# Kernel tuning notes

Measured on AMD Instinct MI355X. Metric: run time of the kernel, lower is better.

Reference implementation:

```python
import jax, jax.numpy as jnp
import numpy as np

B, T, C = 2, 2048, 1024
H = 16
DH = C // H  # 64
DFF = 4 * C  # 4096
EPS = 1e-5


def layernorm(x, gamma, beta):
    # torch.var defaults to unbiased (ddof=1) -- replicate exactly
    m = jnp.mean(x, axis=-1, keepdims=True)
    v = jnp.var(x, axis=-1, ddof=1, keepdims=True)
    return (x - m) / jnp.sqrt(v + EPS) * gamma + beta


def setup_inputs() -> dict:
    key = jax.random.key(0)
    ks = jax.random.split(key, 12)
    s = 0.02
    return {
        "x": jax.random.normal(ks[0], (B, T, C), jnp.float32),
        "Wq": jax.random.normal(ks[1], (H, C, DH), jnp.float32) * s,
        "bq": jnp.zeros((H, DH), jnp.float32),
        "Wk": jax.random.normal(ks[2], (H, C, DH), jnp.float32) * s,
        "bk": jnp.zeros((H, DH), jnp.float32),
        "Wv": jax.random.normal(ks[3], (H, C, DH), jnp.float32) * s,
        "bv": jnp.zeros((H, DH), jnp.float32),
        "Wo": jax.random.normal(ks[4], (C, C), jnp.float32) * s,
        "bo": jnp.zeros((C,), jnp.float32),
        "gamma1": jnp.ones((C,), jnp.float32),
        "beta1": jnp.zeros((C,), jnp.float32),
        "gamma2": jnp.ones((C,), jnp.float32),
        "beta2": jnp.zeros((C,), jnp.float32),
        "W1": jax.random.normal(ks[5], (C, DFF), jnp.float32) * s,
        "b1": jnp.zeros((DFF,), jnp.float32),
        "W2": jax.random.normal(ks[6], (DFF, C), jnp.float32) * s,
        "b2": jnp.zeros((C,), jnp.float32),
    }


def reference(x, Wq, bq, Wk, bk, Wv, bv, Wo, bo,
              gamma1, beta1, gamma2, beta2, W1, b1, W2, b2):
    Tn = x.shape[1]
    # Block: x = ln1(x); x = x + attn(x); x = ln2(x); out = x + ffw(x)
    x = layernorm(x, gamma1, beta1)

    # per-head Q/K/V linears, stacked over heads: [B,T,C] x [H,C,Dh] -> [B,H,T,Dh]
    q = jnp.einsum('btc,hcd->bhtd', x, Wq) + bq[None, :, None, :]
    k = jnp.einsum('btc,hcd->bhtd', x, Wk) + bk[None, :, None, :]
    v = jnp.einsum('btc,hcd->bhtd', x, Wv) + bv[None, :, None, :]

    scale = DH ** -0.5
    scores = jnp.einsum('bhtd,bhsd->bhts', q, k) * scale  # [B,H,T,T]
    causal = jnp.tril(jnp.ones((Tn, Tn), dtype=bool))
    scores = jnp.where(causal, scores, -jnp.inf)
    alpha = jax.nn.softmax(scores, axis=-1)
    h = jnp.einsum('bhts,bhsd->bhtd', alpha, v)  # [B,H,T,Dh]
    h = jnp.transpose(h, (0, 2, 1, 3)).reshape(x.shape)  # concat heads -> [B,T,C]
    attn_out = h @ Wo + bo

    x = x + attn_out
    x = layernorm(x, gamma2, beta2)
    ffw = jax.nn.gelu(x @ W1 + b1, approximate=False) @ W2 + b2
    return x + ffw
```

## Files before the change

### kernel.cpp

```cpp
#include <hip/hip_runtime.h>

typedef unsigned short u16;
typedef unsigned int u32;
typedef __attribute__((ext_vector_type(8))) short bf16x8;
typedef __attribute__((ext_vector_type(4))) float f32x4;

#define AS1 __attribute__((address_space(1)))
#define AS3 __attribute__((address_space(3)))

__device__ __forceinline__ u16 f2bf(float f) {
  u32 u = __float_as_uint(f);
  u = (u + 0x7fffu + ((u >> 16) & 1u)) >> 16;
  return (u16)u;
}
__device__ __forceinline__ float bf2f(u16 v) { return __uint_as_float((u32)v << 16); }

__device__ __forceinline__ void gl16(const void* g, void* l) {
  __builtin_amdgcn_global_load_lds((AS1 void*)g, (AS3 void*)l, 16, 0, 0);
}

__device__ __forceinline__ float exp2a(float x) {
  float r;
  asm("v_exp_f32 %0, %1" : "=v"(r) : "v"(x));
  return r;
}
__device__ __forceinline__ u32 pk2(float lo, float hi) {
  u32 r;
  asm("v_cvt_pk_bf16_f32 %0, %1, %2" : "=v"(r) : "v"(lo), "v"(hi));
  return r;
}

#define LGKM0()                                         \
  do {                                                  \
    asm volatile("s_waitcnt lgkmcnt(0)" ::: "memory");  \
    __builtin_amdgcn_sched_barrier(0);                  \
  } while (0)
#define VMC0()                                          \
  do {                                                  \
    asm volatile("s_waitcnt vmcnt(0)" ::: "memory");    \
    __builtin_amdgcn_sched_barrier(0);                  \
  } while (0)

__global__ __launch_bounds__(256) void ln_kernel(const float* __restrict__ in,
                                                 const float* __restrict__ gamma,
                                                 const float* __restrict__ beta,
                                                 u16* __restrict__ obf,
                                                 float* __restrict__ of32) {
  const int row = blockIdx.x;
  const int tid = threadIdx.x;
  const float* xr = in + (long)row * 1024;
  float4 v = *(const float4*)(xr + tid * 4);
  float s = v.x + v.y + v.z + v.w;
  float sq = v.x * v.x + v.y * v.y + v.z * v.z + v.w * v.w;
#pragma unroll
  for (int off = 1; off < 64; off <<= 1) {
    s += __shfl_xor(s, off);
    sq += __shfl_xor(sq, off);
  }
  __shared__ float rs[4], rq[4];
  const int w = tid >> 6, lane = tid & 63;
  if (lane == 0) { rs[w] = s; rq[w] = sq; }
  __syncthreads();
  s = rs[0] + rs[1] + rs[2] + rs[3];
  sq = rq[0] + rq[1] + rq[2] + rq[3];
  const float mean = s * (1.0f / 1024.0f);
  const float var = (sq - 1024.0f * mean * mean) * (1.0f / 1023.0f);
  const float rstd = rsqrtf(var + 1e-5f);
  float4 g4 = *(const float4*)(gamma + tid * 4);
  float4 b4 = *(const float4*)(beta + tid * 4);
  float o0 = (v.x - mean) * rstd * g4.x + b4.x;
  float o1 = (v.y - mean) * rstd * g4.y + b4.y;
  float o2 = (v.z - mean) * rstd * g4.z + b4.z;
  float o3 = (v.w - mean) * rstd * g4.w + b4.w;
  *(float4*)(of32 + (long)row * 1024 + tid * 4) = make_float4(o0, o1, o2, o3);
  ushort4 ub;
  ub.x = f2bf(o0); ub.y = f2bf(o1); ub.z = f2bf(o2); ub.w = f2bf(o3);
  *(ushort4*)(obf + (long)row * 1024 + tid * 4) = ub;
}

__global__ __launch_bounds__(256) void ln2_fused_kernel(
    const u16* __restrict__ p0, const u16* __restrict__ p1,
    const float* __restrict__ bo, const float* __restrict__ xn,
    const float* __restrict__ gamma, const float* __restrict__ beta,
    u16* __restrict__ obf, float* __restrict__ of32) {
  const int row = blockIdx.x;
  const int tid = threadIdx.x;
  const long i4 = (long)row * 1024 + tid * 4;
  ushort4 a0 = *(const ushort4*)(p0 + i4);
  ushort4 a1 = *(const ushort4*)(p1 + i4);
  float4 xv = *(const float4*)(xn + i4);
  float4 bv = *(const float4*)(bo + tid * 4);
  float y0 = bf2f(a0.x) + bf2f(a1.x) + bv.x + xv.x;
  float y1 = bf2f(a0.y) + bf2f(a1.y) + bv.y + xv.y;
  float y2 = bf2f(a0.z) + bf2f(a1.z) + bv.z + xv.z;
  float y3 = bf2f(a0.w) + bf2f(a1.w) + bv.w + xv.w;
  float s = y0 + y1 + y2 + y3;
  float sq = y0 * y0 + y1 * y1 + y2 * y2 + y3 * y3;
#pragma unroll
  for (int off = 1; off < 64; off <<= 1) {
    s += __shfl_xor(s, off);
    sq += __shfl_xor(sq, off);
  }
  __shared__ float rs[4], rq[4];
  const int w = tid >> 6, lane = tid & 63;
  if (lane == 0) { rs[w] = s; rq[w] = sq; }
  __syncthreads();
  s = rs[0] + rs[1] + rs[2] + rs[3];
  sq = rq[0] + rq[1] + rq[2] + rq[3];
  const float mean = s * (1.0f / 1024.0f);
  const float var = (sq - 1024.0f * mean * mean) * (1.0f / 1023.0f);
  const float rstd = rsqrtf(var + 1e-5f);
  float4 g4 = *(const float4*)(gamma + tid * 4);
  float4 b4 = *(const float4*)(beta + tid * 4);
  float o0 = (y0 - mean) * rstd * g4.x + b4.x;
  float o1 = (y1 - mean) * rstd * g4.y + b4.y;
  float o2 = (y2 - mean) * rstd * g4.z + b4.z;
  float o3 = (y3 - mean) * rstd * g4.w + b4.w;
  *(float4*)(of32 + i4) = make_float4(o0, o1, o2, o3);
  ushort4 ub;
  ub.x = f2bf(o0); ub.y = f2bf(o1); ub.z = f2bf(o2); ub.w = f2bf(o3);
  *(ushort4*)(obf + i4) = ub;
}

__global__ __launch_bounds__(256) void wtrans_kernel(const float* __restrict__ in,
                                                     u16* __restrict__ out,
                                                     int R, int C, int in_rs,
                                                     long in_batch, long out_batch) {
  __shared__ float tile[32][33];
  const float* ip = in + (long)blockIdx.z * in_batch;
  u16* op = out + (long)blockIdx.z * out_batch;
  const int c0 = blockIdx.x * 32, r0 = blockIdx.y * 32;
  const int tx = threadIdx.x, ty = threadIdx.y;
#pragma unroll
  for (int i = 0; i < 4; ++i)
    tile[ty + i * 8][tx] = ip[(long)(r0 + ty + i * 8) * in_rs + c0 + tx];
  __syncthreads();
#pragma unroll
  for (int i = 0; i < 4; ++i)
    op[(long)(c0 + ty + i * 8) * R + r0 + tx] = f2bf(tile[tx][ty + i * 8]);
}

__global__ __launch_bounds__(256) void ffn2_reduce_kernel(const u16* __restrict__ p,
                                                          const float* __restrict__ b2,
                                                          const float* __restrict__ yn,
                                                          float* __restrict__ out) {
  const long i4 = ((long)blockIdx.x * 256 + threadIdx.x) * 4;
  ushort4 p0 = *(const ushort4*)(p + i4);
  ushort4 p1 = *(const ushort4*)(p + 4194304 + i4);
  ushort4 p2 = *(const ushort4*)(p + 8388608 + i4);
  ushort4 p3 = *(const ushort4*)(p + 12582912 + i4);
  float4 rr = *(const float4*)(yn + i4);
  const int nn = (int)(i4 & 1023);
  float4 bb = *(const float4*)(b2 + nn);
  float4 o;
  o.x = bf2f(p0.x) + bf2f(p1.x) + bf2f(p2.x) + bf2f(p3.x) + bb.x + rr.x;
  o.y = bf2f(p0.y) + bf2f(p1.y) + bf2f(p2.y) + bf2f(p3.y) + bb.y + rr.y;
  o.z = bf2f(p0.z) + bf2f(p1.z) + bf2f(p2.z) + bf2f(p3.z) + bb.z + rr.z;
  o.w = bf2f(p0.w) + bf2f(p1.w) + bf2f(p2.w) + bf2f(p3.w) + bb.w + rr.w;
  *(float4*)(out + i4) = o;
}

template <int EPI>
__global__ __launch_bounds__(256, 2) void gemm128_kernel(
    const u16* __restrict__ A, const u16* __restrict__ Bt,
    int K, int nk, int N,
    const float* bias0, const float* bias1, const float* bias2,
    void* out0, void* out1) {
  __shared__ __align__(16) u16 Asm[128 * 64];
  __shared__ __align__(16) u16 Bsm[128 * 64];
  const int tid = threadIdx.x;
  const int lane = tid & 63, w = tid >> 6;
  const int wm = w >> 1, wn = w & 1;
  const int q = lane & 15, g = lane >> 4;
  const long m0 = (long)blockIdx.x * 128;
  const long n0 = (long)blockIdx.y * 128;
  const int bz = blockIdx.z;
  const long koff = (long)bz * (long)nk * 64;

  f32x4 zero4 = {0.f, 0.f, 0.f, 0.f};
  f32x4 acc[4][4];
#pragma unroll
  for (int mi = 0; mi < 4; ++mi)
#pragma unroll
    for (int ni = 0; ni < 4; ++ni) acc[mi][ni] = zero4;

  for (int ks = 0; ks < nk; ++ks) {
    __syncthreads();
    const u16* ga = A + m0 * K + koff + ks * 64;
    const u16* gb = Bt + n0 * K + koff + ks * 64;
    const int base = w * 256;
#pragma unroll
    for (int i = 0; i < 4; ++i) {
      const int idx = base + i * 64 + lane;
      const int row = idx >> 3;
      const int lg = (idx & 7) ^ (row & 7);
      gl16(ga + (long)row * K + lg * 8, Asm + (long)(base + i * 64) * 8);
    }
#pragma unroll
    for (int i = 0; i < 4; ++i) {
      const int idx = base + i * 64 + lane;
      const int row = idx >> 3;
      const int lg = (idx & 7) ^ (row & 7);
      gl16(gb + (long)row * K + lg * 8, Bsm + (long)(base + i * 64) * 8);
    }
    __syncthreads();
#pragma unroll
    for (int half = 0; half < 2; ++half) {
      bf16x8 af[4], bfv[4];
#pragma unroll
      for (int mi = 0; mi < 4; ++mi) {
        const int row = wm * 64 + mi * 16 + q;
        const int ph = (half * 4 + g) ^ (row & 7);
        af[mi] = *(const bf16x8*)(Asm + row * 64 + ph * 8);
      }
#pragma unroll
      for (int ni = 0; ni < 4; ++ni) {
        const int row = wn * 64 + ni * 16 + q;
        const int ph = (half * 4 + g) ^ (row & 7);
        bfv[ni] = *(const bf16x8*)(Bsm + row * 64 + ph * 8);
      }
#pragma unroll
      for (int mi = 0; mi < 4; ++mi)
#pragma unroll
        for (int ni = 0; ni < 4; ++ni)
          acc[mi][ni] = __builtin_amdgcn_mfma_f32_16x16x32_bf16(af[mi], bfv[ni],
                                                                acc[mi][ni], 0, 0, 0);
    }
  }
#pragma unroll
  for (int mi = 0; mi < 4; ++mi) {
#pragma unroll
    for (int ni = 0; ni < 4; ++ni) {
      const long mbase = m0 + wm * 64 + mi * 16 + 4 * g;
      const long n = n0 + wn * 64 + ni * 16 + q;
      f32x4 a = acc[mi][ni];
      if constexpr (EPI == 0) {
        const int sel = (int)(n >> 10);
        const int nn = (int)(n & 1023);
        const float* bp = sel == 0 ? bias0 : (sel == 1 ? bias1 : bias2);
        const float bb2 = bp[nn];
        if (sel < 2) {
          const float sc = (sel == 0) ? 0.18033688011112043f : 1.0f;
          u16* qkp = (u16*)out0;
#pragma unroll
          for (int r = 0; r < 4; ++r)
            qkp[(mbase + r) * 2048 + n] = f2bf((a[r] + bb2) * sc);
        } else {
          const int bI = (int)(mbase >> 11);
          const int t = (int)(mbase & 2047);
          const int hh = nn >> 6, dh = nn & 63;
          ushort4 pk;
          pk.x = f2bf(a[0] + bb2); pk.y = f2bf(a[1] + bb2);
          pk.z = f2bf(a[2] + bb2); pk.w = f2bf(a[3] + bb2);
          *(ushort4*)((u16*)out1 + ((long)((bI * 16 + hh) * 64 + dh)) * 2048 + t) = pk;
        }
      } else if constexpr (EPI == 2) {
        u16* gp = (u16*)out0;
        const float bb2 = bias0[(int)n];
#pragma unroll
        for (int r = 0; r < 4; ++r) {
          const float xg = a[r] + bb2;
          const float ge = 0.5f * xg * (1.0f + erff(xg * 0.70710678118f));
          gp[(mbase + r) * N + n] = f2bf(ge);
        }
      } else {
        u16* pp = (u16*)out0 + (long)bz * 4096 * 1024;
#pragma unroll
        for (int r = 0; r < 4; ++r) pp[(mbase + r) * 1024 + n] = f2bf(a[r]);
      }
    }
  }
}

__device__ __forceinline__ void attn_stage(const u16* kbase, const u16* vtb, int kb,
                                           u16* Kd, u16* Vd, int tid) {
#pragma unroll
  for (int it = 0; it < 2; ++it) {
    const int j = it * 256 + tid;
    const int row = j >> 3;
    const int lg = (j & 7) ^ (row & 7);
    gl16(kbase + (long)(kb * 64 + row) * 2048 + lg * 8, Kd + j * 8);
    gl16(vtb + (long)row * 2048 + kb * 64 + lg * 8, Vd + j * 8);
  }
}

__device__ __forceinline__ void softmax_slab(const f32x4 st[4], bool diag, int qrow,
                                             int kb, int g, int q15,
                                             float& m2, float& l, u16* prow,
                                             float al[4]) {
  float sv[4][4];
  float rmax = -1e30f;
#pragma unroll
  for (int sub = 0; sub < 4; ++sub)
#pragma unroll
    for (int r = 0; r < 4; ++r) {
      float s_ = st[sub][r];
      if (diag) {
        const int key = kb * 64 + sub * 16 + 4 * g + r;
        s_ = (key > qrow) ? -1e30f : s_;
      }
      sv[sub][r] = s_;
      rmax = fmaxf(rmax, s_);
    }
  rmax = fmaxf(rmax, __shfl_xor(rmax, 16));
  rmax = fmaxf(rmax, __shfl_xor(rmax, 32));
  const float mnew = fmaxf(m2, rmax);
  const float alpha = exp2a(m2 - mnew);
  float psum = 0.f;
#pragma unroll
  for (int sub = 0; sub < 4; ++sub) {
    const float p0 = exp2a(sv[sub][0] - mnew);
    const float p1 = exp2a(sv[sub][1] - mnew);
    const float p2 = exp2a(sv[sub][2] - mnew);
    const float p3 = exp2a(sv[sub][3] - mnew);
    uint2 u;
    u.x = pk2(p0, p1);
    u.y = pk2(p2, p3);
    *(uint2*)(prow + sub * 16 + 4 * g) = u;
    psum += (p0 + p1) + (p2 + p3);
  }
  psum += __shfl_xor(psum, 16);
  psum += __shfl_xor(psum, 32);
  l = l * alpha + psum;
  m2 = mnew;
#pragma unroll
  for (int r = 0; r < 4; ++r) al[r] = __shfl(alpha, 4 * g + r);
}

__global__ __launch_bounds__(256, 2) void attn_kernel(const u16* __restrict__ qk,
                                                      const u16* __restrict__ vT,
                                                      u16* __restrict__ o) {
  __shared__ __align__(16) u16 Ksm[2][64 * 64];
  __shared__ __align__(16) u16 Vsm[2][64 * 64];
  __shared__ __align__(16) u16 Psm[8][16][72];
  const int lid = blockIdx.x;
  const int xcd = lid & 7, s6 = lid >> 3;
  const int b2 = (s6 >> 4) & 3, xr = s6 & 15;
  const int qs = (b2 & 2) ? (15 - xr) : xr;
  const int bh = xcd + 8 * b2;
  const int b = bh >> 4, h = bh & 15;
  const int tid = threadIdx.x, lane = tid & 63, w = tid >> 6;
  const int q15 = lane & 15, g = lane >> 4;
  const u16* qbase = qk + (long)b * 2048 * 2048 + h * 64;
  const u16* kbase = qbase + 1024;
  const u16* vtb = vT + (long)bh * 64 * 2048;
  f32x4 zero4 = {0.f, 0.f, 0.f, 0.f};

  const int r0 = qs * 128 + w * 16 + q15;
  bf16x8 qa[2][2];
  qa[0][0] = *(const bf16x8*)(qbase + (long)r0 * 2048 + g * 8);
  qa[0][1] = *(const bf16x8*)(qbase + (long)r0 * 2048 + 32 + g * 8);
  qa[1][0] = *(const bf16x8*)(qbase + (long)(r0 + 64) * 2048 + g * 8);
  qa[1][1] = *(const bf16x8*)(qbase + (long)(r0 + 64) * 2048 + 32 + g * 8);

  f32x4 oa0[4], oa1[4];
#pragma unroll
  for (int dv = 0; dv < 4; ++dv) { oa0[dv] = zero4; oa1[dv] = zero4; }
  float m20 = -1e30f, l0 = 0.f, m21 = -1e30f, l1 = 0.f;
  const int kbmax = 2 * qs + 1;

  attn_stage(kbase, vtb, 0, Ksm[0], Vsm[0], tid);
  VMC0();
  __syncthreads();

  for (int kb = 0; kb <= kbmax; ++kb) {
    const int buf = kb & 1;
    if (kb < kbmax) attn_stage(kbase, vtb, kb + 1, Ksm[buf ^ 1], Vsm[buf ^ 1], tid);
    const u16* Kb = Ksm[buf];
    const u16* Vb = Vsm[buf];
    const bool s0on = (kb <= 2 * qs);
    f32x4 st0[4], st1[4];
#pragma unroll
    for (int sub = 0; sub < 4; ++sub) {
      const int row = sub * 16 + q15;
      const bf16x8 ka0 = *(const bf16x8*)(Kb + row * 64 + ((g ^ (row & 7)) * 8));
      const bf16x8 ka1 = *(const bf16x8*)(Kb + row * 64 + (((4 + g) ^ (row & 7)) * 8));
      f32x4 z = zero4;
      z = __builtin_amdgcn_mfma_f32_16x16x32_bf16(ka0, qa[1][0], z, 0, 0, 0);
      z = __builtin_amdgcn_mfma_f32_16x16x32_bf16(ka1, qa[1][1], z, 0, 0, 0);
      st1[sub] = z;
      if (s0on) {
        f32x4 z0 = zero4;
        z0 = __builtin_amdgcn_mfma_f32_16x16x32_bf16(ka0, qa[0][0], z0, 0, 0, 0);
        z0 = __builtin_amdgcn_mfma_f32_16x16x32_bf16(ka1, qa[0][1], z0, 0, 0, 0);
        st0[sub] = z0;
      }
    }
    float al0[4], al1[4];
    if (s0on)
      softmax_slab(st0, kb == 2 * qs, r0, kb, g, q15, m20, l0, &Psm[w * 2][q15][0], al0);
    softmax_slab(st1, kb == 2 * qs + 1, r0 + 64, kb, g, q15, m21, l1,
                 &Psm[w * 2 + 1][q15][0], al1);
    if (s0on)
#pragma unroll
      for (int dv = 0; dv < 4; ++dv) {
        oa0[dv][0] *= al0[0]; oa0[dv][1] *= al0[1];
        oa0[dv][2] *= al0[2]; oa0[dv][3] *= al0[3];
      }
#pragma unroll
    for (int dv = 0; dv < 4; ++dv) {
      oa1[dv][0] *= al1[0]; oa1[dv][1] *= al1[1];
      oa1[dv][2] *= al1[2]; oa1[dv][3] *= al1[3];
    }
    LGKM0();
#pragma unroll
    for (int half = 0; half < 2; ++half) {
      const bf16x8 pa0 = *(const bf16x8*)(&Psm[w * 2][q15][half * 32 + 8 * g]);
      const bf16x8 pa1 = *(const bf16x8*)(&Psm[w * 2 + 1][q15][half * 32 + 8 * g]);
#pragma unroll
      for (int dv = 0; dv < 4; ++dv) {
        const int row = dv * 16 + q15;
        const bf16x8 vb = *(const bf16x8*)(Vb + row * 64 + (((half * 4 + g) ^ (row & 7)) * 8));
        if (s0on) oa0[dv] = __builtin_amdgcn_mfma_f32_16x16x32_bf16(pa0, vb, oa0[dv], 0, 0, 0);
        oa1[dv] = __builtin_amdgcn_mfma_f32_16x16x32_bf16(pa1, vb, oa1[dv], 0, 0, 0);
      }
    }
    VMC0();
    __syncthreads();
  }
  const float li0 = 1.0f / l0, li1 = 1.0f / l1;
  float v0[4], v1[4];
#pragma unroll
  for (int r = 0; r < 4; ++r) {
    v0[r] = __shfl(li0, 4 * g + r);
    v1[r] = __shfl(li1, 4 * g + r);
  }
  const int tok0 = b * 2048 + qs * 128 + w * 16;
#pragma unroll
  for (int dv = 0; dv < 4; ++dv)
#pragma unroll
    for (int r = 0; r < 4; ++r) {
      o[(long)(tok0 + 4 * g + r) * 1024 + h * 64 + dv * 16 + q15] =
          f2bf(oa0[dv][r] * v0[r]);
      o[(long)(tok0 + 64 + 4 * g + r) * 1024 + h * 64 + dv * 16 + q15] =
          f2bf(oa1[dv][r] * v1[r]);
    }
}

extern "C" void kernel_launch(void* const* d_in, const int* in_sizes, int n_in,
                              void* d_out, int out_size, void* d_ws, size_t ws_size,
                              hipStream_t stream) {
  (void)in_sizes; (void)n_in; (void)out_size; (void)ws_size;
  const float* x  = (const float*)d_in[0];
  const float* Wq = (const float*)d_in[1];
  const float* bq = (const float*)d_in[2];
  const float* Wk = (const float*)d_in[3];
  const float* bk = (const float*)d_in[4];
  const float* Wv = (const float*)d_in[5];
  const float* bv = (const float*)d_in[6];
  const float* Wo = (const float*)d_in[7];
  const float* bo = (const float*)d_in[8];
  const float* g1 = (const float*)d_in[9];
  const float* be1 = (const float*)d_in[10];
  const float* g2 = (const float*)d_in[11];
  const float* be2 = (const float*)d_in[12];
  const float* W1 = (const float*)d_in[13];
  const float* b1 = (const float*)d_in[14];
  const float* W2 = (const float*)d_in[15];
  const float* b2 = (const float*)d_in[16];

  char* ws = (char*)d_ws;
  u16*   xn_bf = (u16*)  (ws + 0);
  float* xn_f  = (float*)(ws + 8388608);
  u16*   WqkvT = (u16*)  (ws + 25165824);
  u16*   WoT   = (u16*)  (ws + 31457280);
  u16*   W1T   = (u16*)  (ws + 33554432);
  u16*   W2T   = (u16*)  (ws + 41943040);
  u16*   qkb   = (u16*)  (ws + 50331648);
  u16*   vTb   = (u16*)  (ws + 67108864);
  u16*   ah    = (u16*)  (ws + 75497472);
  u16*   pwo0  = (u16*)  (ws + 50331648);
  u16*   pwo1  = (u16*)  (ws + 58720256);
  u16*   gbuf  = (u16*)  (ws + 50331648);
  u16*   part  = (u16*)  (ws + 0);
  u16*   yn_bf = (u16*)  (ws + 83886080);
  float* yn_f  = (float*)(ws + 92274688);

  dim3 tb(32, 8), b256(256);
  wtrans_kernel<<<dim3(2, 32, 16), tb, 0, stream>>>(Wq, WqkvT,            1024, 64, 64, 65536l, 65536l);
  wtrans_kernel<<<dim3(2, 32, 16), tb, 0, stream>>>(Wk, WqkvT + 1048576,  1024, 64, 64, 65536l, 65536l);
  wtrans_kernel<<<dim3(2, 32, 16), tb, 0, stream>>>(Wv, WqkvT + 2097152,  1024, 64, 64, 65536l, 65536l);
  wtrans_kernel<<<dim3(32, 32, 1),  tb, 0, stream>>>(Wo, WoT, 1024, 1024, 1024, 0l, 0l);
  wtrans_kernel<<<dim3(128, 32, 1), tb, 0, stream>>>(W1, W1T, 1024, 4096, 4096, 0l, 0l);
  wtrans_kernel<<<dim3(32, 128, 1), tb, 0, stream>>>(W2, W2T, 4096, 1024, 1024, 0l, 0l);
  ln_kernel<<<dim3(4096), b256, 0, stream>>>(x, g1, be1, xn_bf, xn_f);
  gemm128_kernel<0><<<dim3(32, 24, 1), b256, 0, stream>>>(xn_bf, WqkvT, 1024, 16, 3072,
                                                          bq, bk, bv, qkb, vTb);
  attn_kernel<<<dim3(512), b256, 0, stream>>>(qkb, vTb, ah);
  gemm128_kernel<5><<<dim3(32, 8, 2), b256, 0, stream>>>(ah, WoT, 1024, 8, 1024,
                                                         nullptr, nullptr, nullptr, pwo0, nullptr);
  ln2_fused_kernel<<<dim3(4096), b256, 0, stream>>>(pwo0, pwo1, bo, xn_f, g2, be2,
                                                    yn_bf, yn_f);
  gemm128_kernel<2><<<dim3(32, 32, 1), b256, 0, stream>>>(yn_bf, W1T, 1024, 16, 4096,
                                                          b1, nullptr, nullptr, gbuf, nullptr);
  gemm128_kernel<5><<<dim3(32, 8, 4), b256, 0, stream>>>(gbuf, W2T, 4096, 16, 1024,
                                                         nullptr, nullptr, nullptr, part, nullptr);
  ffn2_reduce_kernel<<<dim3(4096), b256, 0, stream>>>(part, b2, yn_f, (float*)d_out);
}
```

Measured before the change: 229.1 us.

## Balance causal attention by splitting query strips across paired KV ranges

Each attention block now processes two partial tasks: the first half of query strip j's KV range and the second half of strip 15-j's range. This gives every block the same number of KV iterations instead of a per-strip count that grows with position. Partial outputs (unnormalized bf16 O plus per-row max and sum) go to workspace, and a new combine kernel merges the two halves with a log-sum-exp rescale. The cost is an extra launch, extra global traffic for the partials, and some added bf16 rounding of the unnormalized accumulators.

```diff
diff --git a/kernel.cpp b/kernel.cpp
--- a/kernel.cpp
+++ b/kernel.cpp
@@ -327,26 +327,15 @@
   for (int r = 0; r < 4; ++r) al[r] = __shfl(alpha, 4 * g + r);
 }
 
-__global__ __launch_bounds__(256, 2) void attn_kernel(const u16* __restrict__ qk,
-                                                      const u16* __restrict__ vT,
-                                                      u16* __restrict__ o) {
-  __shared__ __align__(16) u16 Ksm[2][64 * 64];
-  __shared__ __align__(16) u16 Vsm[2][64 * 64];
-  __shared__ __align__(16) u16 Psm[8][16][72];
-  const int lid = blockIdx.x;
-  const int xcd = lid & 7, s6 = lid >> 3;
-  const int b2 = (s6 >> 4) & 3, xr = s6 & 15;
-  const int qs = (b2 & 2) ? (15 - xr) : xr;
-  const int bh = xcd + 8 * b2;
-  const int b = bh >> 4, h = bh & 15;
-  const int tid = threadIdx.x, lane = tid & 63, w = tid >> 6;
+__device__ __forceinline__ void attn_part(
+    const u16* __restrict__ qbase, const u16* __restrict__ kbase,
+    const u16* __restrict__ vtb, int s, int kb_lo, int kb_hi,
+    u16* __restrict__ Op, float* __restrict__ Mp, float* __restrict__ Lp,
+    u16* Ksm, u16* Vsm, u16 (*Psm)[16][72], int tid) {
+  const int lane = tid & 63, w = tid >> 6;
   const int q15 = lane & 15, g = lane >> 4;
-  const u16* qbase = qk + (long)b * 2048 * 2048 + h * 64;
-  const u16* kbase = qbase + 1024;
-  const u16* vtb = vT + (long)bh * 64 * 2048;
   f32x4 zero4 = {0.f, 0.f, 0.f, 0.f};
-
-  const int r0 = qs * 128 + w * 16 + q15;
+  const int r0 = s * 128 + w * 16 + q15;
   bf16x8 qa[2][2];
   qa[0][0] = *(const bf16x8*)(qbase + (long)r0 * 2048 + g * 8);
   qa[0][1] = *(const bf16x8*)(qbase + (long)r0 * 2048 + 32 + g * 8);
@@ -357,18 +346,18 @@
 #pragma unroll
   for (int dv = 0; dv < 4; ++dv) { oa0[dv] = zero4; oa1[dv] = zero4; }
   float m20 = -1e30f, l0 = 0.f, m21 = -1e30f, l1 = 0.f;
-  const int kbmax = 2 * qs + 1;
-
-  attn_stage(kbase, vtb, 0, Ksm[0], Vsm[0], tid);
+
+  attn_stage(kbase, vtb, kb_lo, Ksm + (kb_lo & 1) * 4096, Vsm + (kb_lo & 1) * 4096, tid);
   VMC0();
   __syncthreads();
 
-  for (int kb = 0; kb <= kbmax; ++kb) {
+  for (int kb = kb_lo; kb <= kb_hi; ++kb) {
     const int buf = kb & 1;
-    if (kb < kbmax) attn_stage(kbase, vtb, kb + 1, Ksm[buf ^ 1], Vsm[buf ^ 1], tid);
-    const u16* Kb = Ksm[buf];
-    const u16* Vb = Vsm[buf];
-    const bool s0on = (kb <= 2 * qs);
+    if (kb < kb_hi)
+      attn_stage(kbase, vtb, kb + 1, Ksm + (buf ^ 1) * 4096, Vsm + (buf ^ 1) * 4096, tid);
+    const u16* Kb = Ksm + buf * 4096;
+    const u16* Vb = Vsm + buf * 4096;
+    const bool s0on = (kb <= 2 * s);
     f32x4 st0[4], st1[4];
 #pragma unroll
     for (int sub = 0; sub < 4; ++sub) {
@@ -388,8 +377,8 @@
     }
     float al0[4], al1[4];
     if (s0on)
-      softmax_slab(st0, kb == 2 * qs, r0, kb, g, q15, m20, l0, &Psm[w * 2][q15][0], al0);
-    softmax_slab(st1, kb == 2 * qs + 1, r0 + 64, kb, g, q15, m21, l1,
+      softmax_slab(st0, kb == 2 * s, r0, kb, g, q15, m20, l0, &Psm[w * 2][q15][0], al0);
+    softmax_slab(st1, kb == 2 * s + 1, r0 + 64, kb, g, q15, m21, l1,
                  &Psm[w * 2 + 1][q15][0], al1);
     if (s0on)
 #pragma unroll
@@ -418,23 +407,81 @@
     VMC0();
     __syncthreads();
   }
-  const float li0 = 1.0f / l0, li1 = 1.0f / l1;
-  float v0[4], v1[4];
-#pragma unroll
-  for (int r = 0; r < 4; ++r) {
-    v0[r] = __shfl(li0, 4 * g + r);
-    v1[r] = __shfl(li1, 4 * g + r);
-  }
-  const int tok0 = b * 2048 + qs * 128 + w * 16;
 #pragma unroll
   for (int dv = 0; dv < 4; ++dv)
 #pragma unroll
     for (int r = 0; r < 4; ++r) {
-      o[(long)(tok0 + 4 * g + r) * 1024 + h * 64 + dv * 16 + q15] =
-          f2bf(oa0[dv][r] * v0[r]);
-      o[(long)(tok0 + 64 + 4 * g + r) * 1024 + h * 64 + dv * 16 + q15] =
-          f2bf(oa1[dv][r] * v1[r]);
-    }
+      Op[(long)(w * 16 + 4 * g + r) * 64 + dv * 16 + q15] = f2bf(oa0[dv][r]);
+      Op[(long)(w * 16 + 64 + 4 * g + r) * 64 + dv * 16 + q15] = f2bf(oa1[dv][r]);
+    }
+  if (g == 0) {
+    Mp[w * 16 + q15] = m20;      Lp[w * 16 + q15] = l0;
+    Mp[w * 16 + 64 + q15] = m21; Lp[w * 16 + 64 + q15] = l1;
+  }
+}
+
+__global__ __launch_bounds__(256, 2) void attn_kernel(const u16* __restrict__ qk,
+                                                      const u16* __restrict__ vT,
+                                                      u16* __restrict__ Op,
+                                                      float* __restrict__ Mp,
+                                                      float* __restrict__ Lp) {
+  __shared__ __align__(16) u16 Ksm[2 * 4096];
+  __shared__ __align__(16) u16 Vsm[2 * 4096];
+  __shared__ __align__(16) u16 Psm[8][16][72];
+  const int lid = blockIdx.x;
+  const int xcd = lid & 7, s6 = lid >> 3;
+  const int b2 = (s6 >> 4) & 3, j = s6 & 15;
+  const int bh = xcd + 8 * b2;
+  const int b = bh >> 4, h = bh & 15;
+  const int tid = threadIdx.x;
+  const u16* qbase = qk + (long)b * 2048 * 2048 + h * 64;
+  const u16* kbase = qbase + 1024;
+  const u16* vtb = vT + (long)bh * 64 * 2048;
+
+  {
+    const long slot = ((long)bh * 16 + j) * 2;
+    attn_part(qbase, kbase, vtb, j, 0, j,
+              Op + slot * 8192, Mp + slot * 128, Lp + slot * 128,
+              Ksm, Vsm, Psm, tid);
+  }
+  {
+    const int s = 15 - j;
+    const long slot = ((long)bh * 16 + s) * 2 + 1;
+    attn_part(qbase, kbase, vtb, s, s + 1, 2 * s + 1,
+              Op + slot * 8192, Mp + slot * 128, Lp + slot * 128,
+              Ksm, Vsm, Psm, tid);
+  }
+}
+
+__global__ __launch_bounds__(256) void attn_combine_kernel(
+    const u16* __restrict__ Op, const float* __restrict__ Mp,
+    const float* __restrict__ Lp, u16* __restrict__ ah) {
+  const int sg = blockIdx.x;
+  const int bh = sg >> 4, s = sg & 15;
+  const int b = bh >> 4, h = bh & 15;
+  const int tid = threadIdx.x;
+  const int r = tid >> 1;
+  const int d0 = (tid & 1) * 32;
+  const long slot = (long)sg * 2;
+  const float mA = Mp[slot * 128 + r], mB = Mp[(slot + 1) * 128 + r];
+  const float lA = Lp[slot * 128 + r], lB = Lp[(slot + 1) * 128 + r];
+  const float m = fmaxf(mA, mB);
+  const float wA = exp2a(mA - m), wB = exp2a(mB - m);
+  const float inv = 1.0f / (lA * wA + lB * wB);
+  const float fA = wA * inv, fB = wB * inv;
+  const u16* pa = Op + slot * 8192 + r * 64 + d0;
+  const u16* pb = Op + (slot + 1) * 8192 + r * 64 + d0;
+  u16* dst = ah + (long)(b * 2048 + s * 128 + r) * 1024 + h * 64 + d0;
+#pragma unroll
+  for (int dd = 0; dd < 32; dd += 8) {
+    bf16x8 va = *(const bf16x8*)(pa + dd);
+    bf16x8 vb = *(const bf16x8*)(pb + dd);
+    bf16x8 ov;
+#pragma unroll
+    for (int e = 0; e < 8; ++e)
+      ov[e] = (short)f2bf(bf2f((u16)va[e]) * fA + bf2f((u16)vb[e]) * fB);
+    *(bf16x8*)(dst + dd) = ov;
+  }
 }
 
 extern "C" void kernel_launch(void* const* d_in, const int* in_sizes, int n_in,
@@ -473,6 +520,9 @@
   u16*   pwo1  = (u16*)  (ws + 58720256);
   u16*   gbuf  = (u16*)  (ws + 50331648);
   u16*   part  = (u16*)  (ws + 0);
+  u16*   aOp   = (u16*)  (ws + 83886080);
+  float* aMp   = (float*)(ws + 100663296);
+  float* aLp   = (float*)(ws + 101187584);
   u16*   yn_bf = (u16*)  (ws + 83886080);
   float* yn_f  = (float*)(ws + 92274688);
 
@@ -486,7 +536,8 @@
   ln_kernel<<<dim3(4096), b256, 0, stream>>>(x, g1, be1, xn_bf, xn_f);
   gemm128_kernel<0><<<dim3(32, 24, 1), b256, 0, stream>>>(xn_bf, WqkvT, 1024, 16, 3072,
                                                           bq, bk, bv, qkb, vTb);
-  attn_kernel<<<dim3(512), b256, 0, stream>>>(qkb, vTb, ah);
+  attn_kernel<<<dim3(512), b256, 0, stream>>>(qkb, vTb, aOp, aMp, aLp);
+  attn_combine_kernel<<<dim3(512), b256, 0, stream>>>(aOp, aMp, aLp, ah);
   gemm128_kernel<5><<<dim3(32, 8, 2), b256, 0, stream>>>(ah, WoT, 1024, 8, 1024,
                                                          nullptr, nullptr, nullptr, pwo0, nullptr);
   ln2_fused_kernel<<<dim3(4096), b256, 0, stream>>>(pwo0, pwo1, bo, xn_f, g2, be2,
```

Result: slower. 241.2 us (+5.3%).

## Load attention K/V tiles directly into registers and merge QKV weight transposes

Applied to the files above, without the earlier changes.

The attention kernel drops its LDS double-buffered K/V staging and the per-tile block barriers. Each lane now loads its K and V MFMA operands straight from global memory into registers, with software prefetch of the next K tile through two ping-ponged register sets. The three Q/K/V weight-transpose launches are merged into one kernel launch to cut launch overhead. The trade-offs are higher register pressure, duplicated global loads across the four waves (served by cache rather than shared memory), and less latency hiding for V, which is loaded in the same tile that uses it.

```diff
diff --git a/kernel.cpp b/kernel.cpp
--- a/kernel.cpp
+++ b/kernel.cpp
@@ -140,6 +140,26 @@
     op[(long)(c0 + ty + i * 8) * R + r0 + tx] = f2bf(tile[tx][ty + i * 8]);
 }
 
+__global__ __launch_bounds__(256) void wtrans3_kernel(const float* __restrict__ Wq,
+                                                      const float* __restrict__ Wk,
+                                                      const float* __restrict__ Wv,
+                                                      u16* __restrict__ out) {
+  __shared__ float tile[32][33];
+  const int z = blockIdx.z;
+  const float* in = z < 16 ? Wq : (z < 32 ? Wk : Wv);
+  const float* ip = in + (long)(z & 15) * 65536;
+  u16* op = out + (long)z * 65536;
+  const int c0 = blockIdx.x * 32, r0 = blockIdx.y * 32;
+  const int tx = threadIdx.x, ty = threadIdx.y;
+#pragma unroll
+  for (int i = 0; i < 4; ++i)
+    tile[ty + i * 8][tx] = ip[(long)(r0 + ty + i * 8) * 64 + c0 + tx];
+  __syncthreads();
+#pragma unroll
+  for (int i = 0; i < 4; ++i)
+    op[(long)(c0 + ty + i * 8) * 1024 + r0 + tx] = f2bf(tile[tx][ty + i * 8]);
+}
+
 __global__ __launch_bounds__(256) void ffn2_reduce_kernel(const u16* __restrict__ p,
                                                           const float* __restrict__ b2,
                                                           const float* __restrict__ yn,
@@ -272,18 +292,6 @@
   }
 }
 
-__device__ __forceinline__ void attn_stage(const u16* kbase, const u16* vtb, int kb,
-                                           u16* Kd, u16* Vd, int tid) {
-#pragma unroll
-  for (int it = 0; it < 2; ++it) {
-    const int j = it * 256 + tid;
-    const int row = j >> 3;
-    const int lg = (j & 7) ^ (row & 7);
-    gl16(kbase + (long)(kb * 64 + row) * 2048 + lg * 8, Kd + j * 8);
-    gl16(vtb + (long)row * 2048 + kb * 64 + lg * 8, Vd + j * 8);
-  }
-}
-
 __device__ __forceinline__ void softmax_slab(const f32x4 st[4], bool diag, int qrow,
                                              int kb, int g, int q15,
                                              float& m2, float& l, u16* prow,
@@ -327,11 +335,64 @@
   for (int r = 0; r < 4; ++r) al[r] = __shfl(alpha, 4 * g + r);
 }
 
+#define LDK(DST, KB)                                                          \
+  _Pragma("unroll") for (int sub = 0; sub < 4; ++sub)                         \
+      _Pragma("unroll") for (int kh = 0; kh < 2; ++kh)                        \
+          DST[sub][kh] = *(const bf16x8*)(kp + ((long)(KB) * 64 + sub * 16) * 2048 + kh * 32);
+
+#define LDV(KB)                                                               \
+  _Pragma("unroll") for (int half = 0; half < 2; ++half)                      \
+      _Pragma("unroll") for (int dv = 0; dv < 4; ++dv)                        \
+          vbr[half][dv] = *(const bf16x8*)(vp + (long)(dv * 16) * 2048 + (KB) * 64 + half * 32);
+
+#define ATILE(CUR, NXT, KB)                                                   \
+  do {                                                                        \
+    LDV(KB);                                                                  \
+    if ((KB) + 1 < nt) LDK(NXT, (KB) + 1);                                    \
+    const bool s0on = ((KB) <= 2 * qs);                                       \
+    f32x4 st0[4], st1[4];                                                     \
+    _Pragma("unroll") for (int sub = 0; sub < 4; ++sub) {                     \
+      f32x4 z = zero4;                                                        \
+      z = __builtin_amdgcn_mfma_f32_16x16x32_bf16(CUR[sub][0], qa[1][0], z, 0, 0, 0); \
+      z = __builtin_amdgcn_mfma_f32_16x16x32_bf16(CUR[sub][1], qa[1][1], z, 0, 0, 0); \
+      st1[sub] = z;                                                           \
+      if (s0on) {                                                             \
+        f32x4 z0 = zero4;                                                     \
+        z0 = __builtin_amdgcn_mfma_f32_16x16x32_bf16(CUR[sub][0], qa[0][0], z0, 0, 0, 0); \
+        z0 = __builtin_amdgcn_mfma_f32_16x16x32_bf16(CUR[sub][1], qa[0][1], z0, 0, 0, 0); \
+        st0[sub] = z0;                                                        \
+      }                                                                       \
+    }                                                                         \
+    float al0[4], al1[4];                                                     \
+    if (s0on)                                                                 \
+      softmax_slab(st0, (KB) == 2 * qs, r0, (KB), g, q15, m20, l0,            \
+                   &Psm[w * 2][q15][0], al0);                                 \
+    softmax_slab(st1, (KB) == 2 * qs + 1, r0 + 64, (KB), g, q15, m21, l1,     \
+                 &Psm[w * 2 + 1][q15][0], al1);                               \
+    if (s0on)                                                                 \
+      _Pragma("unroll") for (int dv = 0; dv < 4; ++dv) {                      \
+        oa0[dv][0] *= al0[0]; oa0[dv][1] *= al0[1];                           \
+        oa0[dv][2] *= al0[2]; oa0[dv][3] *= al0[3];                           \
+      }                                                                       \
+    _Pragma("unroll") for (int dv = 0; dv < 4; ++dv) {                        \
+      oa1[dv][0] *= al1[0]; oa1[dv][1] *= al1[1];                             \
+      oa1[dv][2] *= al1[2]; oa1[dv][3] *= al1[3];                             \
+    }                                                                         \
+    LGKM0();                                                                  \
+    _Pragma("unroll") for (int half = 0; half < 2; ++half) {                  \
+      const bf16x8 pa0 = *(const bf16x8*)(&Psm[w * 2][q15][half * 32 + 8 * g]); \
+      const bf16x8 pa1 = *(const bf16x8*)(&Psm[w * 2 + 1][q15][half * 32 + 8 * g]); \
+      _Pragma("unroll") for (int dv = 0; dv < 4; ++dv) {                      \
+        if (s0on)                                                             \
+          oa0[dv] = __builtin_amdgcn_mfma_f32_16x16x32_bf16(pa0, vbr[half][dv], oa0[dv], 0, 0, 0); \
+        oa1[dv] = __builtin_amdgcn_mfma_f32_16x16x32_bf16(pa1, vbr[half][dv], oa1[dv], 0, 0, 0); \
+      }                                                                       \
+    }                                                                         \
+  } while (0)
+
 __global__ __launch_bounds__(256, 2) void attn_kernel(const u16* __restrict__ qk,
                                                       const u16* __restrict__ vT,
                                                       u16* __restrict__ o) {
-  __shared__ __align__(16) u16 Ksm[2][64 * 64];
-  __shared__ __align__(16) u16 Vsm[2][64 * 64];
   __shared__ __align__(16) u16 Psm[8][16][72];
   const int lid = blockIdx.x;
   const int xcd = lid & 7, s6 = lid >> 3;
@@ -357,67 +418,19 @@
 #pragma unroll
   for (int dv = 0; dv < 4; ++dv) { oa0[dv] = zero4; oa1[dv] = zero4; }
   float m20 = -1e30f, l0 = 0.f, m21 = -1e30f, l1 = 0.f;
-  const int kbmax = 2 * qs + 1;
-
-  attn_stage(kbase, vtb, 0, Ksm[0], Vsm[0], tid);
-  VMC0();
-  __syncthreads();
-
-  for (int kb = 0; kb <= kbmax; ++kb) {
-    const int buf = kb & 1;
-    if (kb < kbmax) attn_stage(kbase, vtb, kb + 1, Ksm[buf ^ 1], Vsm[buf ^ 1], tid);
-    const u16* Kb = Ksm[buf];
-    const u16* Vb = Vsm[buf];
-    const bool s0on = (kb <= 2 * qs);
-    f32x4 st0[4], st1[4];
-#pragma unroll
-    for (int sub = 0; sub < 4; ++sub) {
-      const int row = sub * 16 + q15;
-      const bf16x8 ka0 = *(const bf16x8*)(Kb + row * 64 + ((g ^ (row & 7)) * 8));
-      const bf16x8 ka1 = *(const bf16x8*)(Kb + row * 64 + (((4 + g) ^ (row & 7)) * 8));
-      f32x4 z = zero4;
-      z = __builtin_amdgcn_mfma_f32_16x16x32_bf16(ka0, qa[1][0], z, 0, 0, 0);
-      z = __builtin_amdgcn_mfma_f32_16x16x32_bf16(ka1, qa[1][1], z, 0, 0, 0);
-      st1[sub] = z;
-      if (s0on) {
-        f32x4 z0 = zero4;
-        z0 = __builtin_amdgcn_mfma_f32_16x16x32_bf16(ka0, qa[0][0], z0, 0, 0, 0);
-        z0 = __builtin_amdgcn_mfma_f32_16x16x32_bf16(ka1, qa[0][1], z0, 0, 0, 0);
-        st0[sub] = z0;
-      }
-    }
-    float al0[4], al1[4];
-    if (s0on)
-      softmax_slab(st0, kb == 2 * qs, r0, kb, g, q15, m20, l0, &Psm[w * 2][q15][0], al0);
-    softmax_slab(st1, kb == 2 * qs + 1, r0 + 64, kb, g, q15, m21, l1,
-                 &Psm[w * 2 + 1][q15][0], al1);
-    if (s0on)
-#pragma unroll
-      for (int dv = 0; dv < 4; ++dv) {
-        oa0[dv][0] *= al0[0]; oa0[dv][1] *= al0[1];
-        oa0[dv][2] *= al0[2]; oa0[dv][3] *= al0[3];
-      }
-#pragma unroll
-    for (int dv = 0; dv < 4; ++dv) {
-      oa1[dv][0] *= al1[0]; oa1[dv][1] *= al1[1];
-      oa1[dv][2] *= al1[2]; oa1[dv][3] *= al1[3];
-    }
-    LGKM0();
-#pragma unroll
-    for (int half = 0; half < 2; ++half) {
-      const bf16x8 pa0 = *(const bf16x8*)(&Psm[w * 2][q15][half * 32 + 8 * g]);
-      const bf16x8 pa1 = *(const bf16x8*)(&Psm[w * 2 + 1][q15][half * 32 + 8 * g]);
-#pragma unroll
-      for (int dv = 0; dv < 4; ++dv) {
-        const int row = dv * 16 + q15;
-        const bf16x8 vb = *(const bf16x8*)(Vb + row * 64 + (((half * 4 + g) ^ (row & 7)) * 8));
-        if (s0on) oa0[dv] = __builtin_amdgcn_mfma_f32_16x16x32_bf16(pa0, vb, oa0[dv], 0, 0, 0);
-        oa1[dv] = __builtin_amdgcn_mfma_f32_16x16x32_bf16(pa1, vb, oa1[dv], 0, 0, 0);
-      }
-    }
-    VMC0();
-    __syncthreads();
-  }
+  const int nt = 2 * qs + 2;
+
+  const u16* kp = kbase + (long)q15 * 2048 + g * 8;
+  const u16* vp = vtb + (long)q15 * 2048 + g * 8;
+
+  bf16x8 kaA[4][2], kaB[4][2], vbr[2][4];
+  LDK(kaA, 0);
+
+  for (int t = 0; t < nt; t += 2) {
+    ATILE(kaA, kaB, t);
+    ATILE(kaB, kaA, t + 1);
+  }
+
   const float li0 = 1.0f / l0, li1 = 1.0f / l1;
   float v0[4], v1[4];
 #pragma unroll
@@ -477,9 +490,7 @@
   float* yn_f  = (float*)(ws + 92274688);
 
   dim3 tb(32, 8), b256(256);
-  wtrans_kernel<<<dim3(2, 32, 16), tb, 0, stream>>>(Wq, WqkvT,            1024, 64, 64, 65536l, 65536l);
-  wtrans_kernel<<<dim3(2, 32, 16), tb, 0, stream>>>(Wk, WqkvT + 1048576,  1024, 64, 64, 65536l, 65536l);
-  wtrans_kernel<<<dim3(2, 32, 16), tb, 0, stream>>>(Wv, WqkvT + 2097152,  1024, 64, 64, 65536l, 65536l);
+  wtrans3_kernel<<<dim3(2, 32, 48), tb, 0, stream>>>(Wq, Wk, Wv, WqkvT);
   wtrans_kernel<<<dim3(32, 32, 1),  tb, 0, stream>>>(Wo, WoT, 1024, 1024, 1024, 0l, 0l);
   wtrans_kernel<<<dim3(128, 32, 1), tb, 0, stream>>>(W1, W1T, 1024, 4096, 4096, 0l, 0l);
   wtrans_kernel<<<dim3(32, 128, 1), tb, 0, stream>>>(W2, W2T, 4096, 1024, 1024, 0l, 0l);
```

Measured after the change: 236.5 us. 3.2% more time.

## Split attention into 64-row query tiles with 128-thread blocks; merge QKV transposes

Applied to the files above, without the earlier changes.

The attention kernel now gives each block a 64-query tile handled by 2 waves (128 threads) instead of a 128-query tile handled by 4 waves. The grid doubles to 1024 blocks and causal work is spread more finely across blocks, with load balancing done by reversing the tile index in alternate groups. Each block now loads K/V blocks with half as many threads, so each block reads more K/V traffic relative to its compute. The three Q/K/V weight transposes are also merged into a single launch to cut launch overhead.

```diff
diff --git a/kernel.cpp b/kernel.cpp
--- a/kernel.cpp
+++ b/kernel.cpp
@@ -140,6 +140,26 @@
     op[(long)(c0 + ty + i * 8) * R + r0 + tx] = f2bf(tile[tx][ty + i * 8]);
 }
 
+__global__ __launch_bounds__(256) void wtrans3_kernel(const float* __restrict__ Wq,
+                                                      const float* __restrict__ Wk,
+                                                      const float* __restrict__ Wv,
+                                                      u16* __restrict__ out) {
+  __shared__ float tile[32][33];
+  const int z = blockIdx.z;
+  const float* in = z < 16 ? Wq : (z < 32 ? Wk : Wv);
+  const float* ip = in + (long)(z & 15) * 65536;
+  u16* op = out + (long)z * 65536;
+  const int c0 = blockIdx.x * 32, r0 = blockIdx.y * 32;
+  const int tx = threadIdx.x, ty = threadIdx.y;
+#pragma unroll
+  for (int i = 0; i < 4; ++i)
+    tile[ty + i * 8][tx] = ip[(long)(r0 + ty + i * 8) * 64 + c0 + tx];
+  __syncthreads();
+#pragma unroll
+  for (int i = 0; i < 4; ++i)
+    op[(long)(c0 + ty + i * 8) * 1024 + r0 + tx] = f2bf(tile[tx][ty + i * 8]);
+}
+
 __global__ __launch_bounds__(256) void ffn2_reduce_kernel(const u16* __restrict__ p,
                                                           const float* __restrict__ b2,
                                                           const float* __restrict__ yn,
@@ -272,15 +292,15 @@
   }
 }
 
-__device__ __forceinline__ void attn_stage(const u16* kbase, const u16* vtb, int kb,
-                                           u16* Kd, u16* Vd, int tid) {
-#pragma unroll
-  for (int it = 0; it < 2; ++it) {
-    const int j = it * 256 + tid;
-    const int row = j >> 3;
-    const int lg = (j & 7) ^ (row & 7);
-    gl16(kbase + (long)(kb * 64 + row) * 2048 + lg * 8, Kd + j * 8);
-    gl16(vtb + (long)row * 2048 + kb * 64 + lg * 8, Vd + j * 8);
+__device__ __forceinline__ void attn_stage2(const u16* kbase, const u16* vtb, int kb,
+                                            u16* Kd, u16* Vd, int tid) {
+#pragma unroll
+  for (int it = 0; it < 4; ++it) {
+    const int ji = it * 128 + tid;
+    const int row = ji >> 3;
+    const int lg = (ji & 7) ^ (row & 7);
+    gl16(kbase + (long)(kb * 64 + row) * 2048 + lg * 8, Kd + ji * 8);
+    gl16(vtb + (long)row * 2048 + kb * 64 + lg * 8, Vd + ji * 8);
   }
 }
 
@@ -327,16 +347,18 @@
   for (int r = 0; r < 4; ++r) al[r] = __shfl(alpha, 4 * g + r);
 }
 
-__global__ __launch_bounds__(256, 2) void attn_kernel(const u16* __restrict__ qk,
-                                                      const u16* __restrict__ vT,
-                                                      u16* __restrict__ o) {
-  __shared__ __align__(16) u16 Ksm[2][64 * 64];
-  __shared__ __align__(16) u16 Vsm[2][64 * 64];
-  __shared__ __align__(16) u16 Psm[8][16][72];
+__global__ __launch_bounds__(128) void attn_kernel(const u16* __restrict__ qk,
+                                                   const u16* __restrict__ vT,
+                                                   u16* __restrict__ o) {
+  __shared__ __align__(16) u16 Ksm[2 * 4096];
+  __shared__ __align__(16) u16 Vsm[2 * 4096];
+  __shared__ __align__(16) u16 Psm[4][16][72];
   const int lid = blockIdx.x;
-  const int xcd = lid & 7, s6 = lid >> 3;
-  const int b2 = (s6 >> 4) & 3, xr = s6 & 15;
-  const int qs = (b2 & 2) ? (15 - xr) : xr;
+  const int xcd = lid & 7;
+  const int rest = lid >> 3;
+  const int b2 = rest >> 5;
+  const int j0 = rest & 31;
+  const int j = (b2 & 1) ? (31 - j0) : j0;
   const int bh = xcd + 8 * b2;
   const int b = bh >> 4, h = bh & 15;
   const int tid = threadIdx.x, lane = tid & 63, w = tid >> 6;
@@ -346,59 +368,50 @@
   const u16* vtb = vT + (long)bh * 64 * 2048;
   f32x4 zero4 = {0.f, 0.f, 0.f, 0.f};
 
-  const int r0 = qs * 128 + w * 16 + q15;
+  const int r0 = j * 64 + w * 16 + q15;
   bf16x8 qa[2][2];
   qa[0][0] = *(const bf16x8*)(qbase + (long)r0 * 2048 + g * 8);
   qa[0][1] = *(const bf16x8*)(qbase + (long)r0 * 2048 + 32 + g * 8);
-  qa[1][0] = *(const bf16x8*)(qbase + (long)(r0 + 64) * 2048 + g * 8);
-  qa[1][1] = *(const bf16x8*)(qbase + (long)(r0 + 64) * 2048 + 32 + g * 8);
+  qa[1][0] = *(const bf16x8*)(qbase + (long)(r0 + 32) * 2048 + g * 8);
+  qa[1][1] = *(const bf16x8*)(qbase + (long)(r0 + 32) * 2048 + 32 + g * 8);
 
   f32x4 oa0[4], oa1[4];
 #pragma unroll
   for (int dv = 0; dv < 4; ++dv) { oa0[dv] = zero4; oa1[dv] = zero4; }
   float m20 = -1e30f, l0 = 0.f, m21 = -1e30f, l1 = 0.f;
-  const int kbmax = 2 * qs + 1;
-
-  attn_stage(kbase, vtb, 0, Ksm[0], Vsm[0], tid);
+
+  attn_stage2(kbase, vtb, 0, Ksm, Vsm, tid);
   VMC0();
   __syncthreads();
 
-  for (int kb = 0; kb <= kbmax; ++kb) {
+  for (int kb = 0; kb <= j; ++kb) {
     const int buf = kb & 1;
-    if (kb < kbmax) attn_stage(kbase, vtb, kb + 1, Ksm[buf ^ 1], Vsm[buf ^ 1], tid);
-    const u16* Kb = Ksm[buf];
-    const u16* Vb = Vsm[buf];
-    const bool s0on = (kb <= 2 * qs);
+    if (kb < j)
+      attn_stage2(kbase, vtb, kb + 1, Ksm + (buf ^ 1) * 4096, Vsm + (buf ^ 1) * 4096, tid);
+    const u16* Kb = Ksm + buf * 4096;
+    const u16* Vb = Vsm + buf * 4096;
+    const bool diag = (kb == j);
     f32x4 st0[4], st1[4];
 #pragma unroll
     for (int sub = 0; sub < 4; ++sub) {
       const int row = sub * 16 + q15;
       const bf16x8 ka0 = *(const bf16x8*)(Kb + row * 64 + ((g ^ (row & 7)) * 8));
       const bf16x8 ka1 = *(const bf16x8*)(Kb + row * 64 + (((4 + g) ^ (row & 7)) * 8));
-      f32x4 z = zero4;
-      z = __builtin_amdgcn_mfma_f32_16x16x32_bf16(ka0, qa[1][0], z, 0, 0, 0);
-      z = __builtin_amdgcn_mfma_f32_16x16x32_bf16(ka1, qa[1][1], z, 0, 0, 0);
-      st1[sub] = z;
-      if (s0on) {
-        f32x4 z0 = zero4;
-        z0 = __builtin_amdgcn_mfma_f32_16x16x32_bf16(ka0, qa[0][0], z0, 0, 0, 0);
-        z0 = __builtin_amdgcn_mfma_f32_16x16x32_bf16(ka1, qa[0][1], z0, 0, 0, 0);
-        st0[sub] = z0;
-      }
+      f32x4 z0 = zero4, z1 = zero4;
+      z0 = __builtin_amdgcn_mfma_f32_16x16x32_bf16(ka0, qa[0][0], z0, 0, 0, 0);
+      z0 = __builtin_amdgcn_mfma_f32_16x16x32_bf16(ka1, qa[0][1], z0, 0, 0, 0);
+      st0[sub] = z0;
+      z1 = __builtin_amdgcn_mfma_f32_16x16x32_bf16(ka0, qa[1][0], z1, 0, 0, 0);
+      z1 = __builtin_amdgcn_mfma_f32_16x16x32_bf16(ka1, qa[1][1], z1, 0, 0, 0);
+      st1[sub] = z1;
     }
     float al0[4], al1[4];
-    if (s0on)
-      softmax_slab(st0, kb == 2 * qs, r0, kb, g, q15, m20, l0, &Psm[w * 2][q15][0], al0);
-    softmax_slab(st1, kb == 2 * qs + 1, r0 + 64, kb, g, q15, m21, l1,
-                 &Psm[w * 2 + 1][q15][0], al1);
-    if (s0on)
-#pragma unroll
-      for (int dv = 0; dv < 4; ++dv) {
-        oa0[dv][0] *= al0[0]; oa0[dv][1] *= al0[1];
-        oa0[dv][2] *= al0[2]; oa0[dv][3] *= al0[3];
-      }
+    softmax_slab(st0, diag, r0, kb, g, q15, m20, l0, &Psm[w * 2][q15][0], al0);
+    softmax_slab(st1, diag, r0 + 32, kb, g, q15, m21, l1, &Psm[w * 2 + 1][q15][0], al1);
 #pragma unroll
     for (int dv = 0; dv < 4; ++dv) {
+      oa0[dv][0] *= al0[0]; oa0[dv][1] *= al0[1];
+      oa0[dv][2] *= al0[2]; oa0[dv][3] *= al0[3];
       oa1[dv][0] *= al1[0]; oa1[dv][1] *= al1[1];
       oa1[dv][2] *= al1[2]; oa1[dv][3] *= al1[3];
     }
@@ -411,7 +424,7 @@
       for (int dv = 0; dv < 4; ++dv) {
         const int row = dv * 16 + q15;
         const bf16x8 vb = *(const bf16x8*)(Vb + row * 64 + (((half * 4 + g) ^ (row & 7)) * 8));
-        if (s0on) oa0[dv] = __builtin_amdgcn_mfma_f32_16x16x32_bf16(pa0, vb, oa0[dv], 0, 0, 0);
+        oa0[dv] = __builtin_amdgcn_mfma_f32_16x16x32_bf16(pa0, vb, oa0[dv], 0, 0, 0);
         oa1[dv] = __builtin_amdgcn_mfma_f32_16x16x32_bf16(pa1, vb, oa1[dv], 0, 0, 0);
       }
     }
@@ -425,14 +438,14 @@
     v0[r] = __shfl(li0, 4 * g + r);
     v1[r] = __shfl(li1, 4 * g + r);
   }
-  const int tok0 = b * 2048 + qs * 128 + w * 16;
+  const int tok0 = b * 2048 + j * 64 + w * 16;
 #pragma unroll
   for (int dv = 0; dv < 4; ++dv)
 #pragma unroll
     for (int r = 0; r < 4; ++r) {
       o[(long)(tok0 + 4 * g + r) * 1024 + h * 64 + dv * 16 + q15] =
           f2bf(oa0[dv][r] * v0[r]);
-      o[(long)(tok0 + 64 + 4 * g + r) * 1024 + h * 64 + dv * 16 + q15] =
+      o[(long)(tok0 + 32 + 4 * g + r) * 1024 + h * 64 + dv * 16 + q15] =
           f2bf(oa1[dv][r] * v1[r]);
     }
 }
@@ -477,16 +490,14 @@
   float* yn_f  = (float*)(ws + 92274688);
 
   dim3 tb(32, 8), b256(256);
-  wtrans_kernel<<<dim3(2, 32, 16), tb, 0, stream>>>(Wq, WqkvT,            1024, 64, 64, 65536l, 65536l);
-  wtrans_kernel<<<dim3(2, 32, 16), tb, 0, stream>>>(Wk, WqkvT + 1048576,  1024, 64, 64, 65536l, 65536l);
-  wtrans_kernel<<<dim3(2, 32, 16), tb, 0, stream>>>(Wv, WqkvT + 2097152,  1024, 64, 64, 65536l, 65536l);
+  wtrans3_kernel<<<dim3(2, 32, 48), tb, 0, stream>>>(Wq, Wk, Wv, WqkvT);
   wtrans_kernel<<<dim3(32, 32, 1),  tb, 0, stream>>>(Wo, WoT, 1024, 1024, 1024, 0l, 0l);
   wtrans_kernel<<<dim3(128, 32, 1), tb, 0, stream>>>(W1, W1T, 1024, 4096, 4096, 0l, 0l);
   wtrans_kernel<<<dim3(32, 128, 1), tb, 0, stream>>>(W2, W2T, 4096, 1024, 1024, 0l, 0l);
   ln_kernel<<<dim3(4096), b256, 0, stream>>>(x, g1, be1, xn_bf, xn_f);
   gemm128_kernel<0><<<dim3(32, 24, 1), b256, 0, stream>>>(xn_bf, WqkvT, 1024, 16, 3072,
                                                           bq, bk, bv, qkb, vTb);
-  attn_kernel<<<dim3(512), b256, 0, stream>>>(qkb, vTb, ah);
+  attn_kernel<<<dim3(1024), dim3(128), 0, stream>>>(qkb, vTb, ah);
   gemm128_kernel<5><<<dim3(32, 8, 2), b256, 0, stream>>>(ah, WoT, 1024, 8, 1024,
                                                          nullptr, nullptr, nullptr, pwo0, nullptr);
   ln2_fused_kernel<<<dim3(4096), b256, 0, stream>>>(pwo0, pwo1, bo, xn_f, g2, be2,
```

After: 237.9 us. 3.8% more time.
